# Optimization experiments

Measured on AMD Instinct MI355X. Metric: run time of the kernel, lower is better.

## Reference

```python
import jax, jax.numpy as jnp
import numpy as np

N_NODES = 100000
N_EDGES = 1600000
IN_CH = 128
OUT_CH = 64
HID = 2 * OUT_CH


def setup_inputs() -> dict:
    key = jax.random.key(0)
    ks = jax.random.split(key, 9)
    x = jax.random.normal(ks[0], (N_NODES, IN_CH), dtype=jnp.float32)
    edge_index = jax.random.randint(ks[1], (2, N_EDGES), 0, N_NODES, dtype=jnp.int64)
    s = 0.05
    W1 = jax.random.normal(ks[2], (IN_CH, HID), dtype=jnp.float32) * s
    b1 = jnp.zeros((HID,), dtype=jnp.float32)
    Wmu = jax.random.normal(ks[3], (HID, OUT_CH), dtype=jnp.float32) * s
    bmu = jnp.zeros((OUT_CH,), dtype=jnp.float32)
    Wls = jax.random.normal(ks[4], (HID, OUT_CH), dtype=jnp.float32) * s
    bls = jnp.zeros((OUT_CH,), dtype=jnp.float32)
    eps = jax.random.normal(ks[5], (N_NODES, OUT_CH), dtype=jnp.float32)
    return {"x": x, "edge_index": edge_index, "W1": W1, "b1": b1,
            "Wmu": Wmu, "bmu": bmu, "Wls": Wls, "bls": bls, "eps": eps}


def _gcn_conv(x, W, b, src, dst, dis):
    # PyG GCNConv: out = D^{-1/2}(A+I)D^{-1/2} X W + b, self-loops added.
    h = x @ W  # [N, F]
    norm = dis[src] * dis[dst]  # per-edge symmetric norm
    msg = h[src] * norm[:, None]  # [E, F] gathered + scaled messages
    agg = jax.ops.segment_sum(msg, dst, num_segments=x.shape[0])
    agg = agg + h * (dis * dis)[:, None]  # self-loop term
    return agg + b


def reference(x, edge_index, W1, b1, Wmu, bmu, Wls, bls, eps):
    src, dst = edge_index[0], edge_index[1]
    N = x.shape[0]
    # degree over A + I (aggregation at dst, +1 for self loop)
    deg = jax.ops.segment_sum(jnp.ones_like(dst, dtype=x.dtype), dst,
                              num_segments=N) + 1.0
    dis = jax.lax.rsqrt(deg)  # deg >= 1, safe
    h = _gcn_conv(x, W1, b1, src, dst, dis)
    mu = _gcn_conv(h, Wmu, bmu, src, dst, dis)
    logstd = _gcn_conv(h, Wls, bls, src, dst, dis)
    z = mu + eps * jnp.exp(logstd)  # reparametrization trick
    return (z, mu, logstd)
```

## Files before the change

### kernel.cpp

```cpp
#include <hip/hip_runtime.h>
#include <hip/hip_bf16.h>


typedef unsigned int u32;
typedef unsigned short u16;
typedef unsigned char u8;
typedef __bf16 bf16x8 __attribute__((ext_vector_type(8)));
typedef float f32x4 __attribute__((ext_vector_type(4)));
typedef int i32x4 __attribute__((ext_vector_type(4)));

#define NBKT 196
#define BSH 9

__device__ __forceinline__ u16 f2bf(float f) {
    union { float f; u32 u; } v; v.f = f;
    u32 u = v.u;
    u += 0x7fffu + ((u >> 16) & 1u);
    return (u16)(u >> 16);
}
__device__ __forceinline__ float bflo(u32 p) {
    union { u32 u; float f; } v; v.u = p << 16; return v.f;
}
__device__ __forceinline__ float bfhi(u32 p) {
    union { u32 u; float f; } v; v.u = p & 0xffff0000u; return v.f;
}

__global__ __launch_bounds__(256) void bcount(const int* __restrict__ dst,
                                              u32* __restrict__ bucketCnt, int E) {
    __shared__ u32 hist[NBKT];
    int t = threadIdx.x;
    for (int i = t; i < NBKT; i += 256) hist[i] = 0;
    __syncthreads();
    int base = (blockIdx.x * 256 + t) * 4;
    if (base + 3 < E) {
        i32x4 d4 = __builtin_nontemporal_load((const i32x4*)(dst + base));
        atomicAdd(&hist[d4.x >> BSH], 1u);
        atomicAdd(&hist[d4.y >> BSH], 1u);
        atomicAdd(&hist[d4.z >> BSH], 1u);
        atomicAdd(&hist[d4.w >> BSH], 1u);
    } else {
        for (int i = base; i < E; ++i) atomicAdd(&hist[dst[i] >> BSH], 1u);
    }
    __syncthreads();
    for (int i = t; i < NBKT; i += 256)
        if (hist[i]) atomicAdd(&bucketCnt[i], hist[i]);
}

__global__ __launch_bounds__(256) void bscan(const u32* __restrict__ bucketCnt,
                                             u32* __restrict__ bucketStart,
                                             u32* __restrict__ bucketCur,
                                             u32* __restrict__ rowstart,
                                             int N, int E) {
    __shared__ u32 s[256];
    int t = threadIdx.x;
    u32 v = (t < NBKT) ? bucketCnt[t] : 0u;
    s[t] = v;
    for (int off = 1; off < 256; off <<= 1) {
        __syncthreads();
        u32 add = (t >= off) ? s[t - off] : 0u;
        __syncthreads();
        s[t] += add;
    }
    __syncthreads();
    if (t < NBKT) {
        u32 ex = s[t] - v;
        bucketStart[t] = ex;
        bucketCur[t] = ex;
        if (t == NBKT - 1) bucketStart[NBKT] = s[t];
    }
    if (t == 0) rowstart[N] = (u32)E;
}

__global__ __launch_bounds__(256) void bscatter(const int* __restrict__ src,
                                                const int* __restrict__ dst,
                                                u32* __restrict__ bucketCur,
                                                u32* __restrict__ bksrc,
                                                u32* __restrict__ bkdst, int E) {
    __shared__ u32 hist[NBKT], lstart[NBKT], gbase[NBKT];
    __shared__ u32 sA[256];
    __shared__ u32 stS[1024], stD[1024];
    int t = threadIdx.x;
    int e0 = blockIdx.x * 1024;
    int m = min(1024, E - e0);
    for (int i = t; i < NBKT; i += 256) hist[i] = 0;
    __syncthreads();

    int sv[4], dv[4]; u32 rk[4];
    int base = e0 + t * 4;
    bool vec = (base + 3 < E);
    if (vec) {
        i32x4 s4 = __builtin_nontemporal_load((const i32x4*)(src + base));
        i32x4 d4 = __builtin_nontemporal_load((const i32x4*)(dst + base));
        sv[0] = s4.x; sv[1] = s4.y; sv[2] = s4.z; sv[3] = s4.w;
        dv[0] = d4.x; dv[1] = d4.y; dv[2] = d4.z; dv[3] = d4.w;
#pragma unroll
        for (int j = 0; j < 4; ++j) rk[j] = atomicAdd(&hist[dv[j] >> BSH], 1u);
    } else {
#pragma unroll
        for (int j = 0; j < 4; ++j) {
            if (base + j < E) {
                sv[j] = src[base + j]; dv[j] = dst[base + j];
                rk[j] = atomicAdd(&hist[dv[j] >> BSH], 1u);
            }
        }
    }
    __syncthreads();
    sA[t] = (t < NBKT) ? hist[t] : 0u;
    for (int off = 1; off < 256; off <<= 1) {
        __syncthreads();
        u32 add = (t >= off) ? sA[t - off] : 0u;
        __syncthreads();
        sA[t] += add;
    }
    __syncthreads();
    if (t < NBKT) {
        lstart[t] = sA[t] - hist[t];
        if (hist[t]) gbase[t] = atomicAdd(&bucketCur[t], hist[t]);
    }
    __syncthreads();
#pragma unroll
    for (int j = 0; j < 4; ++j) {
        if (base + j < E) {
            int b = dv[j] >> BSH;
            u32 p = lstart[b] + rk[j];
            stS[p] = (u32)sv[j];
            stD[p] = (u32)dv[j];
        }
    }
    __syncthreads();
    for (int i = t; i < m; i += 256) {
        u32 d = stD[i];
        int b = (int)(d >> BSH);
        u32 g = gbase[b] + ((u32)i - lstart[b]);
        bksrc[g] = stS[i];
        bkdst[g] = d;
    }
}

__global__ __launch_bounds__(512) void bbuild(const u32* __restrict__ bksrc,
                                              const u32* __restrict__ bkdst,
                                              const u32* __restrict__ bucketStart,
                                              u32* __restrict__ rowstart,
                                              float* __restrict__ dis,
                                              int* __restrict__ csr, int N) {
    __shared__ u32 degL[512], exL[512];
    int t = threadIdx.x, b = blockIdx.x;
    int n0 = b << BSH;
    int nn = min(N - n0, 512);
    u32 ebeg = bucketStart[b], eend = bucketStart[b + 1];
    degL[t] = 0;
    __syncthreads();
    for (u32 e = ebeg + t; e < eend; e += 512)
        atomicAdd(&degL[bkdst[e] - (u32)n0], 1u);
    __syncthreads();
    u32 v = degL[t];
    exL[t] = v;
    for (int off = 1; off < 512; off <<= 1) {
        __syncthreads();
        u32 add = (t >= off) ? exL[t - off] : 0u;
        __syncthreads();
        exL[t] += add;
    }
    __syncthreads();
    u32 absbase = ebeg + exL[t] - v;
    if (t < nn) {
        rowstart[n0 + t] = absbase;
        dis[n0 + t] = rsqrtf((float)v + 1.0f);
    }
    __syncthreads();
    exL[t] = absbase;
    __syncthreads();
    for (u32 e = ebeg + t; e < eend; e += 512) {
        u32 ln = bkdst[e] - (u32)n0;
        u32 pos = atomicAdd(&exL[ln], 1u);
        csr[pos] = (int)bksrc[e];
    }
}

__global__ __launch_bounds__(256) void fuse_w(const float* __restrict__ W1,
                                              const float* __restrict__ Wmu,
                                              const float* __restrict__ Wls,
                                              const float* __restrict__ b1,
                                              const float* __restrict__ bmu,
                                              const float* __restrict__ bls,
                                              u16* __restrict__ WfT,
                                              float* __restrict__ bb,
                                              float* __restrict__ bcat) {
    int idx = blockIdx.x * 256 + threadIdx.x;
    if (idx >= 16384) return;
    int k = idx >> 7, n = idx & 127;
    const float* Wcol = (n < 64) ? (Wmu + n) : (Wls + (n - 64));
    float acc = 0.f;
#pragma unroll 8
    for (int j = 0; j < 128; ++j) acc += W1[k * 128 + j] * Wcol[j * 64];
    WfT[n * 128 + k] = f2bf(acc);
    if (k == 0) {
        float accb = 0.f;
#pragma unroll 8
        for (int j = 0; j < 128; ++j) accb += b1[j] * Wcol[j * 64];
        bb[n] = accb;
        bcat[n] = (n < 64) ? bmu[n] : bls[n - 64];
    }
}

__global__ __launch_bounds__(256) void convert_x(const float* __restrict__ x,
                                                 const float* __restrict__ dis,
                                                 u32* __restrict__ xs,
                                                 u32* __restrict__ ts, int N) {
    long i = (long)blockIdx.x * 256 + threadIdx.x;
    long node = i >> 5;
    if (node > N) return;
    if (node == N) {
        ((uint2*)xs)[i] = make_uint2(0u, 0u);
        ((uint2*)ts)[i] = make_uint2(0u, 0u);
        return;
    }
    float dd = dis[node];
    f32x4 v = ((const f32x4*)x)[i];
    u32 p0 = (u32)f2bf(v[0] * dd) | ((u32)f2bf(v[1] * dd) << 16);
    u32 p1 = (u32)f2bf(v[2] * dd) | ((u32)f2bf(v[3] * dd) << 16);
    ((uint2*)xs)[i] = make_uint2(p0, p1);
}

__global__ __launch_bounds__(512) void g1gemm(const u32* __restrict__ xs,
                                              const int* __restrict__ csr,
                                              const u32* __restrict__ rowstart,
                                              const float* __restrict__ dis,
                                              const u16* __restrict__ WfT,
                                              const float* __restrict__ bb,
                                              u16* __restrict__ ts, int N) {
    __shared__ __align__(16) u16 ytile[16][136];
    __shared__ float disS[16];
    int tid = threadIdx.x, blk = blockIdx.x;
    int wave = tid >> 6, lane = tid & 63;
    int nsub = lane >> 5;
    int h = (lane >> 4) & 1;
    int l = lane & 15;
    int nl = wave * 2 + nsub;
    int node = blk * 16 + nl;
    bool live = node < N;
    int nodeC = live ? node : 0;
    float dd = dis[nodeC];
    u32 beg = live ? rowstart[nodeC] : 0u;
    u32 end = live ? rowstart[nodeC + 1] : 0u;
    u32 cut = beg + ((end - beg + 1u) >> 1);
    u32 mybeg = h ? cut : beg;
    u32 myend = h ? end : cut;
    if (tid < 16) disS[tid] = (blk * 16 + tid < N) ? dis[blk * 16 + tid] : 0.f;

    const uint4* xs4 = (const uint4*)xs;
    uint4 selfv = xs4[(long)nodeC * 16 + l];
    bool h0 = (h == 0);
    float a0 = h0 ? bflo(selfv.x) : 0.f, a1 = h0 ? bfhi(selfv.x) : 0.f;
    float a2 = h0 ? bflo(selfv.y) : 0.f, a3 = h0 ? bfhi(selfv.y) : 0.f;
    float a4 = h0 ? bflo(selfv.z) : 0.f, a5 = h0 ? bfhi(selfv.z) : 0.f;
    float a6 = h0 ? bflo(selfv.w) : 0.f, a7 = h0 ? bfhi(selfv.w) : 0.f;

    int sbase = nsub * 32 + h * 16;
    int s = (l < 8 && mybeg + (u32)l < myend) ? csr[mybeg + l] : N;
    for (u32 e0 = mybeg; e0 < myend; e0 += 8) {
        u32 e1 = e0 + 8;
        int sn = (l < 8 && e1 < myend && e1 + (u32)l < myend) ? csr[e1 + l] : N;
        uint4 w[8];
#pragma unroll
        for (int j = 0; j < 8; ++j) {
            int sj = __shfl(s, sbase + j);
            w[j] = xs4[(long)sj * 16 + l];
        }
#pragma unroll
        for (int j = 0; j < 8; ++j) {
            a0 += bflo(w[j].x); a1 += bfhi(w[j].x);
            a2 += bflo(w[j].y); a3 += bfhi(w[j].y);
            a4 += bflo(w[j].z); a5 += bfhi(w[j].z);
            a6 += bflo(w[j].w); a7 += bfhi(w[j].w);
        }
        s = sn;
    }
    a0 += __shfl_xor(a0, 16); a1 += __shfl_xor(a1, 16);
    a2 += __shfl_xor(a2, 16); a3 += __shfl_xor(a3, 16);
    a4 += __shfl_xor(a4, 16); a5 += __shfl_xor(a5, 16);
    a6 += __shfl_xor(a6, 16); a7 += __shfl_xor(a7, 16);

    uint4 o = make_uint4(0u, 0u, 0u, 0u);
    if (live) {
        o.x = (u32)f2bf(a0 * dd) | ((u32)f2bf(a1 * dd) << 16);
        o.y = (u32)f2bf(a2 * dd) | ((u32)f2bf(a3 * dd) << 16);
        o.z = (u32)f2bf(a4 * dd) | ((u32)f2bf(a5 * dd) << 16);
        o.w = (u32)f2bf(a6 * dd) | ((u32)f2bf(a7 * dd) << 16);
    }
    if (h0) *(uint4*)&ytile[nl][l * 8] = o;
    __syncthreads();

    int quad = lane >> 4, mn = l;
    bf16x8 af[4];
#pragma unroll
    for (int kk = 0; kk < 4; ++kk)
        af[kk] = *reinterpret_cast<const bf16x8*>(&ytile[mn][kk * 32 + quad * 8]);

    int col = wave * 16 + mn;
    f32x4 acc = {0.f, 0.f, 0.f, 0.f};
#pragma unroll
    for (int kk = 0; kk < 4; ++kk) {
        bf16x8 bf =
            *reinterpret_cast<const bf16x8*>(&WfT[col * 128 + kk * 32 + quad * 8]);
        acc = __builtin_amdgcn_mfma_f32_16x16x32_bf16(af[kk], bf, acc, 0, 0, 0);
    }
    float bc = bb[col];
#pragma unroll
    for (int r = 0; r < 4; ++r) {
        int row = quad * 4 + r;
        int gn = blk * 16 + row;
        if (gn < N)
            __builtin_nontemporal_store(f2bf((acc[r] + bc) * disS[row]),
                                        ts + (long)gn * 128 + col);
    }
}

__global__ __launch_bounds__(256) void gather2(const u32* __restrict__ ts,
                                               const int* __restrict__ csr,
                                               const u32* __restrict__ rowstart,
                                               const float* __restrict__ dis,
                                               const float* __restrict__ bcat,
                                               const float* __restrict__ eps,
                                               float* __restrict__ out, int N) {
    int tid = threadIdx.x;
    int gw = (blockIdx.x * 256 + tid) >> 6;
    int lane = tid & 63;
    int nsub = lane >> 5, h = (lane >> 4) & 1, l = lane & 15;
    int node = gw * 2 + nsub;
    bool live = node < N;
    int nodeC = live ? node : 0;
    float dd = dis[nodeC];
    u32 beg = live ? rowstart[nodeC] : 0u;
    u32 end = live ? rowstart[nodeC + 1] : 0u;
    u32 cut = beg + ((end - beg + 1u) >> 1);
    u32 mybeg = h ? cut : beg;
    u32 myend = h ? end : cut;
    const uint4* ts4 = (const uint4*)ts;

    uint4 selfv = ts4[(long)nodeC * 16 + l];
    bool h0 = (h == 0);
    float a0 = h0 ? bflo(selfv.x) : 0.f, a1 = h0 ? bfhi(selfv.x) : 0.f;
    float a2 = h0 ? bflo(selfv.y) : 0.f, a3 = h0 ? bfhi(selfv.y) : 0.f;
    float a4 = h0 ? bflo(selfv.z) : 0.f, a5 = h0 ? bfhi(selfv.z) : 0.f;
    float a6 = h0 ? bflo(selfv.w) : 0.f, a7 = h0 ? bfhi(selfv.w) : 0.f;

    int sbase = nsub * 32 + h * 16;
    int s = (l < 8 && mybeg + (u32)l < myend) ? csr[mybeg + l] : N;
    for (u32 e0 = mybeg; e0 < myend; e0 += 8) {
        u32 e1 = e0 + 8;
        int sn = (l < 8 && e1 < myend && e1 + (u32)l < myend) ? csr[e1 + l] : N;
        uint4 w[8];
#pragma unroll
        for (int j = 0; j < 8; ++j) {
            int sj = __shfl(s, sbase + j);
            w[j] = ts4[(long)sj * 16 + l];
        }
#pragma unroll
        for (int j = 0; j < 8; ++j) {
            a0 += bflo(w[j].x); a1 += bfhi(w[j].x);
            a2 += bflo(w[j].y); a3 += bfhi(w[j].y);
            a4 += bflo(w[j].z); a5 += bfhi(w[j].z);
            a6 += bflo(w[j].w); a7 += bfhi(w[j].w);
        }
        s = sn;
    }
    a0 += __shfl_xor(a0, 16); a1 += __shfl_xor(a1, 16);
    a2 += __shfl_xor(a2, 16); a3 += __shfl_xor(a3, 16);
    a4 += __shfl_xor(a4, 16); a5 += __shfl_xor(a5, 16);
    a6 += __shfl_xor(a6, 16); a7 += __shfl_xor(a7, 16);

    int c0 = l * 8;
    f32x4 clo = ((const f32x4*)bcat)[2 * l], chi = ((const f32x4*)bcat)[2 * l + 1];
    float v0 = a0 * dd + clo[0];
    float v1 = a1 * dd + clo[1];
    float v2 = a2 * dd + clo[2];
    float v3 = a3 * dd + clo[3];
    float v4 = a4 * dd + chi[0];
    float v5 = a5 * dd + chi[1];
    float v6 = a6 * dd + chi[2];
    float v7 = a7 * dd + chi[3];

    int srcl = lane + 8;
    float w0 = __shfl(v0, srcl), w1 = __shfl(v1, srcl), w2 = __shfl(v2, srcl),
          w3 = __shfl(v3, srcl), w4 = __shfl(v4, srcl), w5 = __shfl(v5, srcl),
          w6 = __shfl(v6, srcl), w7 = __shfl(v7, srcl);

    if (!live || h != 0) return;
    long NO = (long)N * 64;
    if (l < 8) {
        float* mu = out + NO + (long)node * 64 + c0;
        __builtin_nontemporal_store(f32x4{v0, v1, v2, v3}, (f32x4*)mu);
        __builtin_nontemporal_store(f32x4{v4, v5, v6, v7}, (f32x4*)mu + 1);
        const f32x4* ep = (const f32x4*)(eps + (long)node * 64 + c0);
        f32x4 e0v = __builtin_nontemporal_load(ep);
        f32x4 e1v = __builtin_nontemporal_load(ep + 1);
        float* z = out + (long)node * 64 + c0;
        f32x4 z0 = {v0 + e0v[0] * __expf(w0), v1 + e0v[1] * __expf(w1),
                    v2 + e0v[2] * __expf(w2), v3 + e0v[3] * __expf(w3)};
        f32x4 z1 = {v4 + e1v[0] * __expf(w4), v5 + e1v[1] * __expf(w5),
                    v6 + e1v[2] * __expf(w6), v7 + e1v[3] * __expf(w7)};
        __builtin_nontemporal_store(z0, (f32x4*)z);
        __builtin_nontemporal_store(z1, (f32x4*)z + 1);
    } else {
        float* ls = out + 2 * NO + (long)node * 64 + (c0 - 64);
        __builtin_nontemporal_store(f32x4{v0, v1, v2, v3}, (f32x4*)ls);
        __builtin_nontemporal_store(f32x4{v4, v5, v6, v7}, (f32x4*)ls + 1);
    }
}

extern "C" void kernel_launch(void* const* d_in, const int* in_sizes, int n_in,
                              void* d_out, int out_size, void* d_ws, size_t ws_size,
                              hipStream_t stream) {
    const float* x   = (const float*)d_in[0];
    const int* ei    = (const int*)d_in[1];
    const float* W1  = (const float*)d_in[2];
    const float* b1  = (const float*)d_in[3];
    const float* Wmu = (const float*)d_in[4];
    const float* bmu = (const float*)d_in[5];
    const float* Wls = (const float*)d_in[6];
    const float* bls = (const float*)d_in[7];
    const float* eps = (const float*)d_in[8];
    float* out = (float*)d_out;

    const int N = in_sizes[0] / 128;
    const int E = in_sizes[1] / 2;
    const int* src = ei;
    const int* dst = ei + E;

    char* ws = (char*)d_ws;
    u32* rowstart   = (u32*)(ws + 401408);
    u32* bucketCnt  = (u32*)(ws + 802816);
    u32* bucketStart= (u32*)(ws + 804864);
    float* dis      = (float*)(ws + 806912);
    u16* WfT        = (u16*)(ws + 1208320);
    float* bb       = (float*)(ws + 1241088);
    float* bcat     = (float*)(ws + 1241600);
    u32* bucketCur  = (u32*)(ws + 1242112);
    int* csr        = (int*)(ws + 2842112);
    u32* xs         = (u32*)(ws + 9242112);
    u32* ts         = (u32*)(ws + 34842368);
    u32* bksrc      = (u32*)(ws + 34842368);
    u32* bkdst      = (u32*)(ws + 41242368);

    hipMemsetAsync(bucketCnt, 0, 1024, stream);

    int gridE4 = (E / 4 + 255) / 256;
    bcount<<<gridE4, 256, 0, stream>>>(dst, bucketCnt, E);
    bscan<<<1, 256, 0, stream>>>(bucketCnt, bucketStart, bucketCur, rowstart, N, E);
    bscatter<<<gridE4, 256, 0, stream>>>(src, dst, bucketCur, bksrc, bkdst, E);
    bbuild<<<NBKT, 512, 0, stream>>>(bksrc, bkdst, bucketStart, rowstart, dis,
                                     csr, N);

    fuse_w<<<64, 256, 0, stream>>>(W1, Wmu, Wls, b1, bmu, bls, WfT, bb, bcat);

    long Qc = (long)(N + 1) * 32;
    convert_x<<<(int)((Qc + 255) / 256), 256, 0, stream>>>(x, dis, xs, ts, N);

    int gridT = (N + 15) / 16;
    g1gemm<<<gridT, 512, 0, stream>>>(xs, csr, rowstart, dis, WfT, bb,
                                      (u16*)ts, N);

    int gridG = (((N + 1) / 2 + 3) / 4);
    gather2<<<gridG, 256, 0, stream>>>(ts, csr, rowstart, dis, bcat, eps, out, N);
}
```

Before: 390.4 us.

## Embed self-loops in CSR and split gather kernels into two half launches

The CSR build now inserts each node's self-loop as the first entry of its row, so degree includes the self-loop and the gather kernels no longer load the self row separately. Both the aggregation-GEMM and the final gather are launched as two half-range launches with a node offset. The workspace layout is also repacked. This removes special-case self-loop code, but adds one more edge per row and an extra kernel launch per stage.

```diff
diff --git a/kernel.cpp b/kernel.cpp
--- a/kernel.cpp
+++ b/kernel.cpp
@@ -68,7 +68,7 @@
         bucketCur[t] = ex;
         if (t == NBKT - 1) bucketStart[NBKT] = s[t];
     }
-    if (t == 0) rowstart[N] = (u32)E;
+    if (t == 0) rowstart[N] = (u32)(E + N);
 }
 
 __global__ __launch_bounds__(256) void bscatter(const int* __restrict__ src,
@@ -148,12 +148,13 @@
     int n0 = b << BSH;
     int nn = min(N - n0, 512);
     u32 ebeg = bucketStart[b], eend = bucketStart[b + 1];
+    u32 cbase = ebeg + ((u32)b << BSH);
     degL[t] = 0;
     __syncthreads();
     for (u32 e = ebeg + t; e < eend; e += 512)
         atomicAdd(&degL[bkdst[e] - (u32)n0], 1u);
     __syncthreads();
-    u32 v = degL[t];
+    u32 v = degL[t] + ((t < nn) ? 1u : 0u);
     exL[t] = v;
     for (int off = 1; off < 512; off <<= 1) {
         __syncthreads();
@@ -162,13 +163,14 @@
         exL[t] += add;
     }
     __syncthreads();
-    u32 absbase = ebeg + exL[t] - v;
+    u32 rowbase = cbase + exL[t] - v;
     if (t < nn) {
-        rowstart[n0 + t] = absbase;
-        dis[n0 + t] = rsqrtf((float)v + 1.0f);
-    }
-    __syncthreads();
-    exL[t] = absbase;
+        rowstart[n0 + t] = rowbase;
+        dis[n0 + t] = rsqrtf((float)v);
+        csr[rowbase] = n0 + t;
+    }
+    __syncthreads();
+    exL[t] = rowbase + 1;
     __syncthreads();
     for (u32 e = ebeg + t; e < eend; e += 512) {
         u32 ln = bkdst[e] - (u32)n0;
@@ -228,7 +230,8 @@
                                               const float* __restrict__ dis,
                                               const u16* __restrict__ WfT,
                                               const float* __restrict__ bb,
-                                              u16* __restrict__ ts, int N) {
+                                              u16* __restrict__ ts, int N,
+                                              int nodeBase) {
     __shared__ __align__(16) u16 ytile[16][136];
     __shared__ float disS[16];
     int tid = threadIdx.x, blk = blockIdx.x;
@@ -237,7 +240,7 @@
     int h = (lane >> 4) & 1;
     int l = lane & 15;
     int nl = wave * 2 + nsub;
-    int node = blk * 16 + nl;
+    int node = nodeBase + blk * 16 + nl;
     bool live = node < N;
     int nodeC = live ? node : 0;
     float dd = dis[nodeC];
@@ -246,15 +249,13 @@
     u32 cut = beg + ((end - beg + 1u) >> 1);
     u32 mybeg = h ? cut : beg;
     u32 myend = h ? end : cut;
-    if (tid < 16) disS[tid] = (blk * 16 + tid < N) ? dis[blk * 16 + tid] : 0.f;
+    if (tid < 16)
+        disS[tid] = (nodeBase + blk * 16 + tid < N) ? dis[nodeBase + blk * 16 + tid]
+                                                    : 0.f;
 
     const uint4* xs4 = (const uint4*)xs;
-    uint4 selfv = xs4[(long)nodeC * 16 + l];
-    bool h0 = (h == 0);
-    float a0 = h0 ? bflo(selfv.x) : 0.f, a1 = h0 ? bfhi(selfv.x) : 0.f;
-    float a2 = h0 ? bflo(selfv.y) : 0.f, a3 = h0 ? bfhi(selfv.y) : 0.f;
-    float a4 = h0 ? bflo(selfv.z) : 0.f, a5 = h0 ? bfhi(selfv.z) : 0.f;
-    float a6 = h0 ? bflo(selfv.w) : 0.f, a7 = h0 ? bfhi(selfv.w) : 0.f;
+    float a0 = 0.f, a1 = 0.f, a2 = 0.f, a3 = 0.f;
+    float a4 = 0.f, a5 = 0.f, a6 = 0.f, a7 = 0.f;
 
     int sbase = nsub * 32 + h * 16;
     int s = (l < 8 && mybeg + (u32)l < myend) ? csr[mybeg + l] : N;
@@ -288,7 +289,7 @@
         o.z = (u32)f2bf(a4 * dd) | ((u32)f2bf(a5 * dd) << 16);
         o.w = (u32)f2bf(a6 * dd) | ((u32)f2bf(a7 * dd) << 16);
     }
-    if (h0) *(uint4*)&ytile[nl][l * 8] = o;
+    if (h == 0) *(uint4*)&ytile[nl][l * 8] = o;
     __syncthreads();
 
     int quad = lane >> 4, mn = l;
@@ -309,7 +310,7 @@
 #pragma unroll
     for (int r = 0; r < 4; ++r) {
         int row = quad * 4 + r;
-        int gn = blk * 16 + row;
+        int gn = nodeBase + blk * 16 + row;
         if (gn < N)
             __builtin_nontemporal_store(f2bf((acc[r] + bc) * disS[row]),
                                         ts + (long)gn * 128 + col);
@@ -322,12 +323,13 @@
                                                const float* __restrict__ dis,
                                                const float* __restrict__ bcat,
                                                const float* __restrict__ eps,
-                                               float* __restrict__ out, int N) {
+                                               float* __restrict__ out, int N,
+                                               int nodeBase) {
     int tid = threadIdx.x;
     int gw = (blockIdx.x * 256 + tid) >> 6;
     int lane = tid & 63;
     int nsub = lane >> 5, h = (lane >> 4) & 1, l = lane & 15;
-    int node = gw * 2 + nsub;
+    int node = nodeBase + gw * 2 + nsub;
     bool live = node < N;
     int nodeC = live ? node : 0;
     float dd = dis[nodeC];
@@ -338,12 +340,8 @@
     u32 myend = h ? end : cut;
     const uint4* ts4 = (const uint4*)ts;
 
-    uint4 selfv = ts4[(long)nodeC * 16 + l];
-    bool h0 = (h == 0);
-    float a0 = h0 ? bflo(selfv.x) : 0.f, a1 = h0 ? bfhi(selfv.x) : 0.f;
-    float a2 = h0 ? bflo(selfv.y) : 0.f, a3 = h0 ? bfhi(selfv.y) : 0.f;
-    float a4 = h0 ? bflo(selfv.z) : 0.f, a5 = h0 ? bfhi(selfv.z) : 0.f;
-    float a6 = h0 ? bflo(selfv.w) : 0.f, a7 = h0 ? bfhi(selfv.w) : 0.f;
+    float a0 = 0.f, a1 = 0.f, a2 = 0.f, a3 = 0.f;
+    float a4 = 0.f, a5 = 0.f, a6 = 0.f, a7 = 0.f;
 
     int sbase = nsub * 32 + h * 16;
     int s = (l < 8 && mybeg + (u32)l < myend) ? csr[mybeg + l] : N;
@@ -429,19 +427,19 @@
     const int* dst = ei + E;
 
     char* ws = (char*)d_ws;
-    u32* rowstart   = (u32*)(ws + 401408);
-    u32* bucketCnt  = (u32*)(ws + 802816);
-    u32* bucketStart= (u32*)(ws + 804864);
-    float* dis      = (float*)(ws + 806912);
-    u16* WfT        = (u16*)(ws + 1208320);
-    float* bb       = (float*)(ws + 1241088);
-    float* bcat     = (float*)(ws + 1241600);
-    u32* bucketCur  = (u32*)(ws + 1242112);
-    int* csr        = (int*)(ws + 2842112);
-    u32* xs         = (u32*)(ws + 9242112);
-    u32* ts         = (u32*)(ws + 34842368);
-    u32* bksrc      = (u32*)(ws + 34842368);
-    u32* bkdst      = (u32*)(ws + 41242368);
+    u32* rowstart    = (u32*)(ws + 0);
+    u32* bucketCnt   = (u32*)(ws + 401408);
+    u32* bucketStart = (u32*)(ws + 403456);
+    u32* bucketCur   = (u32*)(ws + 405504);
+    float* dis       = (float*)(ws + 407552);
+    u16* WfT         = (u16*)(ws + 808960);
+    float* bb        = (float*)(ws + 841728);
+    float* bcat      = (float*)(ws + 842240);
+    int* csr         = (int*)(ws + 843776);
+    u32* xs          = (u32*)(ws + 7644160);
+    u32* ts          = (u32*)(ws + 33244416);
+    u32* bksrc       = (u32*)(ws + 33244416);
+    u32* bkdst       = (u32*)(ws + 39644416);
 
     hipMemsetAsync(bucketCnt, 0, 1024, stream);
 
@@ -457,10 +455,18 @@
     long Qc = (long)(N + 1) * 32;
     convert_x<<<(int)((Qc + 255) / 256), 256, 0, stream>>>(x, dis, xs, ts, N);
 
-    int gridT = (N + 15) / 16;
-    g1gemm<<<gridT, 512, 0, stream>>>(xs, csr, rowstart, dis, WfT, bb,
-                                      (u16*)ts, N);
-
-    int gridG = (((N + 1) / 2 + 3) / 4);
-    gather2<<<gridG, 256, 0, stream>>>(ts, csr, rowstart, dis, bcat, eps, out, N);
-}
+    int H = (N + 1) / 2;
+    int gridT1 = (H + 15) / 16;
+    int gridT2 = (N - H + 15) / 16;
+    g1gemm<<<gridT1, 512, 0, stream>>>(xs, csr, rowstart, dis, WfT, bb,
+                                       (u16*)ts, N, 0);
+    g1gemm<<<gridT2, 512, 0, stream>>>(xs, csr, rowstart, dis, WfT, bb,
+                                       (u16*)ts, N, H);
+
+    int gridG1 = (H + 7) / 8;
+    int gridG2 = (N - H + 7) / 8;
+    gather2<<<gridG1, 256, 0, stream>>>(ts, csr, rowstart, dis, bcat, eps, out,
+                                        N, 0);
+    gather2<<<gridG2, 256, 0, stream>>>(ts, csr, rowstart, dis, bcat, eps, out,
+                                        N, H);
+}
```

Measured after the change: 408.5 us. 4.6% more time.
